# Kernel optimization log

Measured on AMD Instinct MI355X. Metric: run time of the kernel, lower is better.

Reference implementation:

```python
import jax, jax.numpy as jnp
import numpy as np

T_STEP, NUM_PATCHES = 16, 49
DIM, MLP_DIM, HEADS, DEPTH = 512, 2048, 8, 4
PATCH_DIM = 432
N_BATCH = 32
NEG = -1e9
EPS = 1e-5


def _ln(x, g, b):
    m = x.mean(-1, keepdims=True)
    v = ((x - m) ** 2).mean(-1, keepdims=True)
    return (x - m) / jnp.sqrt(v + EPS) * g + b


def setup_inputs() -> dict:
    key = jax.random.key(0)
    ks = jax.random.split(key, 16)
    L = T_STEP * NUM_PATCHES
    s = 0.02
    return {
        "patch": jax.random.normal(ks[0], (N_BATCH, L, PATCH_DIM), jnp.float32),
        "done": jax.random.randint(ks[1], (N_BATCH, T_STEP - 1), 0, 2).astype(jnp.int32),
        "W_embed": jax.random.normal(ks[2], (PATCH_DIM, DIM), jnp.float32) * s,
        "b_embed": jnp.zeros((DIM,), jnp.float32),
        "spatial_embed": jax.random.normal(ks[3], (1, NUM_PATCHES, DIM), jnp.float32),
        "temporal_embed": jax.random.normal(ks[4], (1, T_STEP, DIM), jnp.float32),
        "ln1_g": jnp.ones((DEPTH, DIM), jnp.float32),
        "ln1_b": jnp.zeros((DEPTH, DIM), jnp.float32),
        "Wqkv": jax.random.normal(ks[5], (DEPTH, DIM, 3 * DIM), jnp.float32) * s,
        "bqkv": jnp.zeros((DEPTH, 3 * DIM), jnp.float32),
        "Wo": jax.random.normal(ks[6], (DEPTH, DIM, DIM), jnp.float32) * s,
        "bo": jnp.zeros((DEPTH, DIM), jnp.float32),
        "ln2_g": jnp.ones((DEPTH, DIM), jnp.float32),
        "ln2_b": jnp.zeros((DEPTH, DIM), jnp.float32),
        "W1": jax.random.normal(ks[7], (DEPTH, DIM, MLP_DIM), jnp.float32) * s,
        "b1": jnp.zeros((DEPTH, MLP_DIM), jnp.float32),
        "W2": jax.random.normal(ks[8], (DEPTH, MLP_DIM, DIM), jnp.float32) * s,
        "b2": jnp.zeros((DEPTH, DIM), jnp.float32),
        "out_g": jnp.ones((DIM,), jnp.float32),
        "out_b": jnp.zeros((DIM,), jnp.float32),
    }


def reference(patch, done, W_embed, b_embed, spatial_embed, temporal_embed,
              ln1_g, ln1_b, Wqkv, bqkv, Wo, bo, ln2_g, ln2_b,
              W1, b1, W2, b2, out_g, out_b):
    N, L, _ = patch.shape
    # patch embed + factored pos embed
    x = patch @ W_embed + b_embed
    pos = jnp.tile(spatial_embed, (1, T_STEP, 1)) + jnp.repeat(temporal_embed, NUM_PATCHES, axis=1)
    x = x + pos
    # episodic attention mask: done_mask[n,t] = 1 iff any done[n, c]==1 for c >= t
    d = done.astype(jnp.float32)  # (N, T-1)
    dm = (jnp.flip(jnp.cumsum(jnp.flip(d, 1), 1), 1) > 0).astype(jnp.float32)
    dm = jnp.concatenate([dm, jnp.zeros((N, 1), jnp.float32)], axis=1)  # (N, T)
    pm = jnp.repeat(dm, NUM_PATCHES, axis=1)  # (N, L)
    keep = 1.0 - pm
    mask = 1.0 - keep[:, :, None] * keep[:, None, :]  # (N, L, L); 1 = blocked
    bias = jnp.where(mask > 0.5, NEG, 0.0)[:, None, :, :]  # (N, 1, L, L)
    dh = DIM // HEADS
    scale = dh ** -0.5
    for i in range(DEPTH):
        h = _ln(x, ln1_g[i], ln1_b[i])
        qkv = h @ Wqkv[i] + bqkv[i]
        q, k, v = jnp.split(qkv, 3, axis=-1)
        q = q.reshape(N, L, HEADS, dh).transpose(0, 2, 1, 3)
        k = k.reshape(N, L, HEADS, dh).transpose(0, 2, 1, 3)
        v = v.reshape(N, L, HEADS, dh).transpose(0, 2, 1, 3)
        scores = jnp.einsum('nhqd,nhkd->nhqk', q, k) * scale + bias
        attn = jax.nn.softmax(scores, axis=-1)
        o = jnp.einsum('nhqk,nhkd->nhqd', attn, v)
        o = o.transpose(0, 2, 1, 3).reshape(N, L, DIM)
        x = x + (o @ Wo[i] + bo[i])
        h = _ln(x, ln2_g[i], ln2_b[i])
        x = x + (jax.nn.gelu(h @ W1[i] + b1[i], approximate=False) @ W2[i] + b2[i])
    return _ln(x, out_g, out_b)
```

## Files before the change

### kernel.cpp

```cpp
#include <hip/hip_runtime.h>
#include <math.h>

#define NB 32
#define LQ 784
#define LQP 832
#define DIM 512
#define HEADS 8
#define MLP 2048
#define KPAD 448
#define MROWS 25088

typedef __attribute__((ext_vector_type(8))) short s8v;
typedef __attribute__((ext_vector_type(4))) short s4v;
typedef __attribute__((ext_vector_type(4))) float f4v;

__device__ __forceinline__ short f2b(float f){
  unsigned u = __builtin_bit_cast(unsigned, f);
  u = (u + 0x7fffu + ((u >> 16) & 1u)) >> 16;
  return (short)u;
}
__device__ __forceinline__ float b2f(short s){
  unsigned u = ((unsigned)(unsigned short)s) << 16;
  return __builtin_bit_cast(float, u);
}

__device__ __forceinline__ void gll16(const short* g, short* l){
  __builtin_amdgcn_global_load_lds(
      (const __attribute__((address_space(1))) void*)g,
      (__attribute__((address_space(3))) void*)l, 16, 0, 0);
}

__global__ __launch_bounds__(512) void mask_k(const int* __restrict__ done, float* __restrict__ keepL,
                                              int* __restrict__ kmask, int* __restrict__ liveg){
  __shared__ float keep[32][16];
  int tid = threadIdx.x;
  { int n = tid >> 4, t = tid & 15;
    int any = 0;
    for (int c = t; c < 15; ++c) any |= done[n*15 + c];
    keep[n][t] = any ? 0.f : 1.f; }
  __syncthreads();
  for (int i = tid; i < NB*LQP; i += 512){
    int n = i / LQP, l = i - n*LQP;
    keepL[i] = (l < LQ) ? keep[n][l/49] : 0.f;
  }
  if (tid < 32){
    int n = tid, m = 0;
    for (int kb = 0; kb < 13; ++kb){
      int t0 = (kb*64)/49, t1 = (kb*64 + 63)/49; if (t1 > 15) t1 = 15;
      float a = 0.f;
      for (int t = t0; t <= t1; ++t) a += keep[n][t];
      if (a > 0.5f) m |= 1 << kb;
    }
    kmask[n] = m;
  }
  for (int g = tid; g < 392; g += 512){
    float a = 0.f;
    for (int i2 = 0; i2 < 64; ++i2){
      int row = g*64 + i2;
      int n = row / 784, l = row - n*784;
      a += keep[n][l/49];
    }
    liveg[g] = a > 0.5f ? 1 : 0;
  }
}

__global__ __launch_bounds__(256) void zpad_k(short* __restrict__ Qb, short* __restrict__ Kb,
                                              short* __restrict__ Vtb){
  int idx = blockIdx.x*256 + threadIdx.x;
  s8v z;
  #pragma unroll
  for (int e=0;e<8;++e) z[e] = 0;
  if (idx < 98304){
    int nh = idx / 384, r = idx - nh*384;
    *(s8v*)(Qb + (long)nh*LQP*64 + 784*64 + r*8) = z;
  } else if (idx < 196608){
    int i2 = idx - 98304; int nh = i2 / 384, r = i2 - nh*384;
    *(s8v*)(Kb + (long)nh*LQP*64 + 784*64 + r*8) = z;
  } else {
    int i2 = idx - 196608; int nh = i2 / 384, rem = i2 - nh*384, d = rem/6, s = rem - d*6;
    *(s8v*)(Vtb + ((long)nh*64 + d)*LQP + 784 + s*8) = z;
  }
}

__global__ __launch_bounds__(256) void vmean_k(const short* __restrict__ Vtb, float* __restrict__ Vm){
  int nh = blockIdx.x;
  int tid = threadIdx.x;
  int d = tid >> 2, seg = tid & 3;
  const short* row = Vtb + ((long)nh*64 + d)*LQP;
  float s = 0.f;
  for (int c = seg; c < 98; c += 4){
    s8v v = *(const s8v*)(row + c*8);
    #pragma unroll
    for (int e=0;e<8;++e) s += b2f(v[e]);
  }
  s += __shfl_xor(s, 1, 64);
  s += __shfl_xor(s, 2, 64);
  if (seg == 0) Vm[nh*64 + d] = s * (1.0f/784.0f);
}

__device__ __forceinline__ void transp_body(long idx, const float* __restrict__ src,
                                            short* __restrict__ dst, int R, int C, int Rpad,
                                            long sStride, long dStride){
  long per = (long)C * Rpad;
  int z = (int)(idx / per);
  long rem = idx - (long)z * per;
  int cc = (int)(rem / Rpad);
  int r  = (int)(rem - (long)cc * Rpad);
  short v = 0;
  if (r < R) v = f2b(src[(long)z * sStride + (long)r * C + cc]);
  dst[(long)z * dStride + rem] = v;
}

#define PB0 43904
#define PB1 896
#define PB2 12288
#define PB3 4096
#define PB4 16384
#define PB5 16384

__global__ __launch_bounds__(256) void prep_k(
    const float* __restrict__ patch, short* __restrict__ patchb,
    const float* __restrict__ Wemb, short* __restrict__ Wembt,
    const float* __restrict__ Wqkv, short* __restrict__ Wqkvt,
    const float* __restrict__ Wo, short* __restrict__ Wot,
    const float* __restrict__ W1, short* __restrict__ W1t,
    const float* __restrict__ W2, short* __restrict__ W2t){
  int b = blockIdx.x;
  int tid = threadIdx.x;
  if (b < PB0){
    long idx = (long)b*256 + tid;
    if (idx >= (long)MROWS*KPAD) return;
    int r = (int)(idx / KPAD);
    int c = (int)(idx - (long)r*KPAD);
    patchb[idx] = (c < 432) ? f2b(patch[(long)r*432 + c]) : (short)0;
  } else if (b < PB0+PB1){
    long idx = (long)(b-PB0)*256 + tid;
    if (idx < 229376) transp_body(idx, Wemb, Wembt, 432, 512, 448, 0, 0);
  } else if (b < PB0+PB1+PB2){
    long idx = (long)(b-PB0-PB1)*256 + tid;
    if (idx < 3145728) transp_body(idx, Wqkv, Wqkvt, 512, 1536, 512, 512L*1536, 1536L*512);
  } else if (b < PB0+PB1+PB2+PB3){
    long idx = (long)(b-PB0-PB1-PB2)*256 + tid;
    if (idx < 1048576) transp_body(idx, Wo, Wot, 512, 512, 512, 512L*512, 512L*512);
  } else if (b < PB0+PB1+PB2+PB3+PB4){
    long idx = (long)(b-PB0-PB1-PB2-PB3)*256 + tid;
    if (idx < 4194304) transp_body(idx, W1, W1t, 512, 2048, 512, 512L*2048, 2048L*512);
  } else {
    long idx = (long)(b-PB0-PB1-PB2-PB3-PB4)*256 + tid;
    if (idx < 4194304) transp_body(idx, W2, W2t, 2048, 512, 2048, 2048L*512, 512L*2048);
  }
}

__global__ __launch_bounds__(256) void ln_k(const float* __restrict__ x, const float* __restrict__ g,
                                            const float* __restrict__ b, short* __restrict__ outb,
                                            float* __restrict__ outf){
  int lane = threadIdx.x & 63;
  long row = (long)blockIdx.x * 4 + (threadIdx.x >> 6);
  const float* xr = x + row * DIM + lane * 8;
  float va[8];
  { float4 t0 = *(const float4*)xr; float4 t1 = *(const float4*)(xr + 4);
    va[0]=t0.x; va[1]=t0.y; va[2]=t0.z; va[3]=t0.w;
    va[4]=t1.x; va[5]=t1.y; va[6]=t1.z; va[7]=t1.w; }
  float s = 0.f, q = 0.f;
  #pragma unroll
  for (int j=0;j<8;++j){ s += va[j]; q += va[j]*va[j]; }
  #pragma unroll
  for (int m=1;m<64;m<<=1){ s += __shfl_xor(s,m,64); q += __shfl_xor(q,m,64); }
  float mean = s * (1.0f/DIM);
  float var = q * (1.0f/DIM) - mean*mean;
  float inv = rsqrtf(var + 1e-5f);
  int cb = lane*8;
  if (outb){
    s8v o;
    #pragma unroll
    for (int j=0;j<8;++j) o[j] = f2b((va[j]-mean)*inv*g[cb+j] + b[cb+j]);
    *(s8v*)(outb + row*DIM + cb) = o;
  } else {
    float4 t0, t1;
    t0.x=(va[0]-mean)*inv*g[cb+0]+b[cb+0]; t0.y=(va[1]-mean)*inv*g[cb+1]+b[cb+1];
    t0.z=(va[2]-mean)*inv*g[cb+2]+b[cb+2]; t0.w=(va[3]-mean)*inv*g[cb+3]+b[cb+3];
    t1.x=(va[4]-mean)*inv*g[cb+4]+b[cb+4]; t1.y=(va[5]-mean)*inv*g[cb+5]+b[cb+5];
    t1.z=(va[6]-mean)*inv*g[cb+6]+b[cb+6]; t1.w=(va[7]-mean)*inv*g[cb+7]+b[cb+7];
    *(float4*)(outf + row*DIM + cb) = t0;
    *(float4*)(outf + row*DIM + cb + 4) = t1;
  }
}

template<int EPI>
__global__ __launch_bounds__(256) void gemm_k(
    const short* __restrict__ A, const short* __restrict__ Bt,
    const float* __restrict__ bias, int K, int N,
    float* __restrict__ xres, short* __restrict__ outb,
    const float* __restrict__ sp, const float* __restrict__ tp)
{
  __shared__ __align__(16) short lA[2][128*64];
  __shared__ __align__(16) short lB[2][128*64];
  long bm = blockIdx.y, bn = blockIdx.x;
  int tid = threadIdx.x;
  int lane = tid & 63, wid = tid >> 6;
  int col = lane & 15, quad = lane >> 4;
  int wm = (wid >> 1) * 64, wn = (wid & 1) * 64;
  f4v acc[4][4];
  #pragma unroll
  for (int i=0;i<4;++i)
    #pragma unroll
    for (int j=0;j<4;++j)
      #pragma unroll
      for (int e=0;e<4;++e) acc[i][j][e] = 0.0f;
  const short* Abase = A + bm*128*(long)K;
  const short* Bbase = Bt + bn*128*(long)K;
  int nt = K >> 6;
  #pragma unroll
  for (int c = 0; c < 4; ++c){
    int v = c*256 + tid;
    int r = v >> 3, j = v & 7;
    int kc = (j ^ (r & 7)) * 8;
    gll16(Abase + (long)r*K + kc, lA[0] + v*8);
    gll16(Bbase + (long)r*K + kc, lB[0] + v*8);
  }
  for (int t = 0; t < nt; ++t){
    int cur = t & 1;
    __builtin_amdgcn_s_barrier();
    __builtin_amdgcn_sched_barrier(0);
    if (t + 1 < nt){
      int kt = (t + 1) << 6;
      #pragma unroll
      for (int c = 0; c < 4; ++c){
        int v = c*256 + tid;
        int r = v >> 3, j = v & 7;
        int kc = (j ^ (r & 7)) * 8;
        gll16(Abase + (long)r*K + kt + kc, lA[cur^1] + v*8);
        gll16(Bbase + (long)r*K + kt + kc, lB[cur^1] + v*8);
      }
      asm volatile("s_waitcnt vmcnt(8)" ::: "memory");
    } else {
      asm volatile("s_waitcnt vmcnt(0)" ::: "memory");
    }
    __builtin_amdgcn_s_barrier();
    __builtin_amdgcn_sched_barrier(0);
    __builtin_amdgcn_s_setprio(1);
    #pragma unroll
    for (int ks = 0; ks < 2; ++ks){
      s8v af[4], bf[4];
      #pragma unroll
      for (int j=0;j<4;++j)
        af[j] = *(const s8v*)&lA[cur][(wm + j*16 + col)*64 + (((ks*4+quad) ^ (col&7)))*8];
      #pragma unroll
      for (int i=0;i<4;++i)
        bf[i] = *(const s8v*)&lB[cur][(wn + i*16 + col)*64 + (((ks*4+quad) ^ (col&7)))*8];
      #pragma unroll
      for (int i=0;i<4;++i)
        #pragma unroll
        for (int j=0;j<4;++j)
          acc[i][j] = __builtin_amdgcn_mfma_f32_16x16x32_bf16(bf[i], af[j], acc[i][j], 0, 0, 0);
    }
    __builtin_amdgcn_s_setprio(0);
    __builtin_amdgcn_sched_barrier(0);
  }
  #pragma unroll
  for (int j=0;j<4;++j){
    int grow = (int)bm*128 + wm + j*16 + col;
    int l = 0, t = 0, p = 0;
    if (EPI == 0){ l = grow % LQ; t = l / 49; p = l - t*49; }
    #pragma unroll
    for (int i=0;i<4;++i){
      int gc0 = (int)bn*128 + wn + i*16 + quad*4;
      float4 b4 = *(const float4*)(bias + gc0);
      float v0 = acc[i][j][0] + b4.x;
      float v1 = acc[i][j][1] + b4.y;
      float v2 = acc[i][j][2] + b4.z;
      float v3 = acc[i][j][3] + b4.w;
      if (EPI == 0){
        float4 s4 = *(const float4*)(sp + p*DIM + gc0);
        float4 t4 = *(const float4*)(tp + t*DIM + gc0);
        float4 o; o.x = v0 + s4.x + t4.x; o.y = v1 + s4.y + t4.y;
        o.z = v2 + s4.z + t4.z; o.w = v3 + s4.w + t4.w;
        *(float4*)(xres + (long)grow*DIM + gc0) = o;
      } else {
        float4 xo = *(const float4*)(xres + (long)grow*DIM + gc0);
        xo.x += v0; xo.y += v1; xo.z += v2; xo.w += v3;
        *(float4*)(xres + (long)grow*DIM + gc0) = xo;
      }
    }
  }
}

template<int EPI>
__global__ __launch_bounds__(512) void gemm256_k(
    const short* __restrict__ A, const short* __restrict__ Bt,
    const float* __restrict__ bias, int K, int N,
    short* __restrict__ outb,
    short* __restrict__ Qb, short* __restrict__ Kb, short* __restrict__ Vtb,
    const int* __restrict__ liveg)
{
  __shared__ __align__(16) short lA[2][256*64];
  __shared__ __align__(16) short lB[2][256*64];
  long bm = blockIdx.y, bn = blockIdx.x;
  if (EPI == 1){
    if (bn < 4 && liveg[4*bm] == 0 && liveg[4*bm+1] == 0 &&
        liveg[4*bm+2] == 0 && liveg[4*bm+3] == 0) return;
  }
  int tid = threadIdx.x;
  int lane = tid & 63, wid = tid >> 6;
  int col = lane & 15, quad = lane >> 4;
  int wm = (wid >> 2) * 128;
  int wn = (wid & 3) * 64;
  f4v acc[4][8];
  #pragma unroll
  for (int i=0;i<4;++i)
    #pragma unroll
    for (int j=0;j<8;++j)
      #pragma unroll
      for (int e=0;e<4;++e) acc[i][j][e] = 0.0f;
  const short* Abase = A + bm*256*(long)K;
  const short* Bbase = Bt + bn*256*(long)K;
  int nt = K >> 6;
  #pragma unroll
  for (int c = 0; c < 4; ++c){
    int v = c*512 + tid;
    int r = v >> 3, j = v & 7;
    int kc = (j ^ (r & 7)) * 8;
    gll16(Abase + (long)r*K + kc, lA[0] + v*8);
    gll16(Bbase + (long)r*K + kc, lB[0] + v*8);
  }
  for (int t = 0; t < nt; ++t){
    int cur = t & 1;
    __builtin_amdgcn_s_barrier();
    __builtin_amdgcn_sched_barrier(0);
    if (t + 1 < nt){
      int kt = (t + 1) << 6;
      #pragma unroll
      for (int c = 0; c < 4; ++c){
        int v = c*512 + tid;
        int r = v >> 3, j = v & 7;
        int kc = (j ^ (r & 7)) * 8;
        gll16(Abase + (long)r*K + kt + kc, lA[cur^1] + v*8);
        gll16(Bbase + (long)r*K + kt + kc, lB[cur^1] + v*8);
      }
      asm volatile("s_waitcnt vmcnt(8)" ::: "memory");
    } else {
      asm volatile("s_waitcnt vmcnt(0)" ::: "memory");
    }
    __builtin_amdgcn_s_barrier();
    __builtin_amdgcn_sched_barrier(0);
    __builtin_amdgcn_s_setprio(1);
    #pragma unroll
    for (int ks = 0; ks < 2; ++ks){
      s8v af[8], bf[4];
      #pragma unroll
      for (int j=0;j<8;++j)
        af[j] = *(const s8v*)&lA[cur][(wm + j*16 + col)*64 + (((ks*4+quad) ^ (col&7)))*8];
      #pragma unroll
      for (int i=0;i<4;++i)
        bf[i] = *(const s8v*)&lB[cur][(wn + i*16 + col)*64 + (((ks*4+quad) ^ (col&7)))*8];
      #pragma unroll
      for (int i=0;i<4;++i)
        #pragma unroll
        for (int j=0;j<8;++j)
          acc[i][j] = __builtin_amdgcn_mfma_f32_16x16x32_bf16(bf[i], af[j], acc[i][j], 0, 0, 0);
    }
    __builtin_amdgcn_s_setprio(0);
    __builtin_amdgcn_sched_barrier(0);
  }
  #pragma unroll
  for (int j=0;j<8;++j){
    int grow = (int)bm*256 + wm + j*16 + col;
    int n = 0, l = 0;
    if (EPI == 1){ n = grow / LQ; l = grow - n*LQ; }
    #pragma unroll
    for (int i=0;i<4;++i){
      int gc0 = (int)bn*256 + wn + i*16 + quad*4;
      float4 b4 = *(const float4*)(bias + gc0);
      float v0 = acc[i][j][0] + b4.x;
      float v1 = acc[i][j][1] + b4.y;
      float v2 = acc[i][j][2] + b4.z;
      float v3 = acc[i][j][3] + b4.w;
      if (EPI == 1){
        if (gc0 < 512){
          int hh = gc0 >> 6, d0 = gc0 & 63;
          s4v o; o[0]=f2b(v0); o[1]=f2b(v1); o[2]=f2b(v2); o[3]=f2b(v3);
          *(s4v*)(Qb + (((long)(n*HEADS + hh))*LQP + l)*64 + d0) = o;
        } else if (gc0 < 1024){
          int c2 = gc0 - 512; int hh = c2 >> 6, d0 = c2 & 63;
          s4v o; o[0]=f2b(v0); o[1]=f2b(v1); o[2]=f2b(v2); o[3]=f2b(v3);
          *(s4v*)(Kb + (((long)(n*HEADS + hh))*LQP + l)*64 + d0) = o;
        } else {
          int c2 = gc0 - 1024; int hh = c2 >> 6, d0 = c2 & 63;
          long base = ((long)(n*HEADS + hh))*64;
          Vtb[(base + d0+0)*LQP + l] = f2b(v0);
          Vtb[(base + d0+1)*LQP + l] = f2b(v1);
          Vtb[(base + d0+2)*LQP + l] = f2b(v2);
          Vtb[(base + d0+3)*LQP + l] = f2b(v3);
        }
      } else {
        float g0 = v0 / (1.0f + __expf(-1.595769122f * v0 * (1.0f + 0.044715f*v0*v0)));
        float g1 = v1 / (1.0f + __expf(-1.595769122f * v1 * (1.0f + 0.044715f*v1*v1)));
        float g2 = v2 / (1.0f + __expf(-1.595769122f * v2 * (1.0f + 0.044715f*v2*v2)));
        float g3 = v3 / (1.0f + __expf(-1.595769122f * v3 * (1.0f + 0.044715f*v3*v3)));
        s4v o; o[0]=f2b(g0); o[1]=f2b(g1); o[2]=f2b(g2); o[3]=f2b(g3);
        *(s4v*)(outb + (long)grow*MLP + gc0) = o;
      }
    }
  }
}

__global__ __launch_bounds__(256) void attn_k(
    const short* __restrict__ Qb, const short* __restrict__ Kb,
    const short* __restrict__ Vtb, const float* __restrict__ keepL,
    const int* __restrict__ kmask, const float* __restrict__ Vm,
    short* __restrict__ Ob)
{
  __shared__ __align__(16) short lK[64*64];
  __shared__ __align__(16) short lV[64*64];
  __shared__ __align__(16) short lP[4][16*72];
  int tid = threadIdx.x;
  int lane = tid & 63, wid = tid >> 6;
  int col = lane & 15, quad = lane >> 4;
  int qb = blockIdx.x, h = blockIdx.y, n = blockIdx.z;
  long nh = (long)n*HEADS + h;
  int smask = kmask[n];
  int qr0 = qb*64 + wid*16;
  float vmv[4];
  #pragma unroll
  for (int j=0;j<4;++j) vmv[j] = Vm[nh*64 + j*16 + col];

  if (!((smask >> qb) & 1)){
    #pragma unroll
    for (int j=0;j<4;++j){
      short ov = f2b(vmv[j]);
      #pragma unroll
      for (int r=0;r<4;++r){
        int l = qr0 + quad*4 + r;
        if (l < LQ) Ob[((long)n*LQ + l)*DIM + h*64 + j*16 + col] = ov;
      }
    }
    return;
  }

  const float* kl = keepL + n*LQP;
  const short* qp = Qb + (nh*LQP + qr0 + col)*64 + quad*8;
  s8v aq0 = *(const s8v*)qp;
  s8v aq1 = *(const s8v*)(qp + 32);
  float keepA = kl[qr0 + col];
  if (keepA < 0.5f){
    #pragma unroll
    for (int e=0;e<8;++e){ aq0[e] = 0; aq1[e] = 0; }
  }
  float keepQ[4];
  #pragma unroll
  for (int r=0;r<4;++r) keepQ[r] = kl[qr0 + quad*4 + r];
  float kqs = keepQ[0] + keepQ[1] + keepQ[2] + keepQ[3];
  bool wlive = __ballot(kqs > 0.5f) != 0ull;
  float lsum[4] = {0.f,0.f,0.f,0.f};
  f4v Oacc[4];
  #pragma unroll
  for (int j=0;j<4;++j)
    #pragma unroll
    for (int e=0;e<4;++e) Oacc[j][e] = 0.0f;

  for (int kb = 0; kb < 13; ++kb){
    if (!((smask >> kb) & 1)) continue;
    int kbase = kb*64;
    __syncthreads();
    #pragma unroll
    for (int c = 0; c < 2; ++c){
      int v = c*256 + tid;
      int r = v >> 3, j = v & 7;
      int kc = (j ^ (r & 7)) * 8;
      gll16(Kb + (nh*LQP + kbase + r)*64 + kc, lK + v*8);
    }
    #pragma unroll
    for (int c = 0; c < 2; ++c){
      int v = c*256 + tid;
      int d = v >> 3, j = v & 7;
      int c8 = (j ^ (d & 7)) * 8;
      gll16(Vtb + (nh*64 + d)*LQP + kbase + c8, lV + v*8);
    }
    __syncthreads();
    if (!wlive) continue;
    float pm[4][4];
    #pragma unroll
    for (int ct = 0; ct < 4; ++ct){
      float keepK = kl[kbase + ct*16 + col];
      f4v s;
      #pragma unroll
      for (int e=0;e<4;++e) s[e] = 0.0f;
      #pragma unroll
      for (int ks = 0; ks < 2; ++ks){
        s8v bk = *(const s8v*)&lK[(ct*16 + col)*64 + (((ks*4+quad) ^ (col&7)))*8];
        if (keepK < 0.5f){
          #pragma unroll
          for (int e=0;e<8;++e) bk[e] = 0;
        }
        s = __builtin_amdgcn_mfma_f32_16x16x32_bf16(ks ? aq1 : aq0, bk, s, 0, 0, 0);
      }
      #pragma unroll
      for (int r=0;r<4;++r){
        float a = keepQ[r] * keepK;
        float t = fmaf(s[r], 0.125f, 10000.0f);
        float p = __expf(fmaf(a, t, -10000.0f));
        pm[ct][r] = p;
        lsum[r] += p;
      }
    }
    #pragma unroll
    for (int ct=0; ct<4; ++ct)
      #pragma unroll
      for (int r=0;r<4;++r)
        lP[wid][(quad*4 + r)*72 + ct*16 + col] = f2b(pm[ct][r]);
    #pragma unroll
    for (int j=0;j<4;++j){
      #pragma unroll
      for (int ks=0; ks<2; ++ks){
        s8v ap = *(const s8v*)&lP[wid][col*72 + ks*32 + quad*8];
        s8v bv = *(const s8v*)&lV[(j*16 + col)*64 + (((ks*4+quad) ^ (col&7)))*8];
        Oacc[j] = __builtin_amdgcn_mfma_f32_16x16x32_bf16(ap, bv, Oacc[j], 0, 0, 0);
      }
    }
  }
  #pragma unroll
  for (int m=1; m<16; m<<=1){
    #pragma unroll
    for (int r=0;r<4;++r) lsum[r] += __shfl_xor(lsum[r], m, 64);
  }
  float invl[4];
  #pragma unroll
  for (int r=0;r<4;++r) invl[r] = 1.0f / lsum[r];
  #pragma unroll
  for (int j=0;j<4;++j)
    #pragma unroll
    for (int r=0;r<4;++r){
      int l = qr0 + quad*4 + r;
      if (l < LQ){
        float val = keepQ[r] > 0.5f ? Oacc[j][r] * invl[r] : vmv[j];
        Ob[((long)n*LQ + l)*DIM + h*64 + j*16 + col] = f2b(val);
      }
    }
}

extern "C" void kernel_launch(void* const* d_in, const int* in_sizes, int n_in,
                              void* d_out, int out_size, void* d_ws, size_t ws_size,
                              hipStream_t stream) {
  const float* patch    = (const float*)d_in[0];
  const int*   done     = (const int*)d_in[1];
  const float* W_embed  = (const float*)d_in[2];
  const float* b_embed  = (const float*)d_in[3];
  const float* spatial  = (const float*)d_in[4];
  const float* temporal = (const float*)d_in[5];
  const float* ln1_g    = (const float*)d_in[6];
  const float* ln1_b    = (const float*)d_in[7];
  const float* Wqkv     = (const float*)d_in[8];
  const float* bqkv     = (const float*)d_in[9];
  const float* Wo       = (const float*)d_in[10];
  const float* bo       = (const float*)d_in[11];
  const float* ln2_g    = (const float*)d_in[12];
  const float* ln2_b    = (const float*)d_in[13];
  const float* W1       = (const float*)d_in[14];
  const float* b1       = (const float*)d_in[15];
  const float* W2       = (const float*)d_in[16];
  const float* b2       = (const float*)d_in[17];
  const float* out_g    = (const float*)d_in[18];
  const float* out_b    = (const float*)d_in[19];
  float* out = (float*)d_out;

  char* ws = (char*)d_ws;
  size_t off = 0;
  auto alloc = [&](size_t bytes)->char*{ char* p = ws + off; off += (bytes + 255) & ~(size_t)255; return p; };
  const size_t QKV_B = (size_t)NB*HEADS*LQP*64*2;
  float* x    = (float*)alloc((size_t)MROWS*DIM*4);
  short* hbuf = (short*)alloc((size_t)MROWS*DIM*2);
  char*  U    = alloc((size_t)MROWS*MLP*2);
  short* patchb = (short*)U;
  short* Qb   = (short*)U;
  short* Kbf  = (short*)(U + QKV_B);
  short* Vtb  = (short*)(U + 2*QKV_B);
  short* obuf = hbuf;
  short* mid  = (short*)U;
  short* Wembt = (short*)alloc((size_t)512*448*2);
  short* Wqkvt = (short*)alloc((size_t)4*1536*512*2);
  short* Wot   = (short*)alloc((size_t)4*512*512*2);
  short* W1t   = (short*)alloc((size_t)4*2048*512*2);
  short* W2t   = (short*)alloc((size_t)4*512*2048*2);
  float* keepL = (float*)alloc((size_t)NB*LQP*4);
  int*   kmask = (int*)alloc(NB*4);
  int*   liveg = (int*)alloc(392*4);
  float* Vm    = (float*)alloc((size_t)NB*HEADS*64*4);

  mask_k<<<1, 512, 0, stream>>>(done, keepL, kmask, liveg);
  prep_k<<<PB0+PB1+PB2+PB3+PB4+PB5, 256, 0, stream>>>(
      patch, patchb, W_embed, Wembt, Wqkv, Wqkvt, Wo, Wot, W1, W1t, W2, W2t);

  gemm_k<0><<<dim3(DIM/128, MROWS/128), 256, 0, stream>>>(
      patchb, Wembt, b_embed, KPAD, DIM, x, nullptr, spatial, temporal);

  zpad_k<<<1152, 256, 0, stream>>>(Qb, Kbf, Vtb);

  for (int i = 0; i < 4; ++i){
    ln_k<<<MROWS/4, 256, 0, stream>>>(x, ln1_g + i*DIM, ln1_b + i*DIM, hbuf, nullptr);
    gemm256_k<1><<<dim3(1536/256, MROWS/256), 512, 0, stream>>>(
        hbuf, Wqkvt + (size_t)i*1536*512, bqkv + (size_t)i*1536, DIM, 1536,
        nullptr, Qb, Kbf, Vtb, liveg);
    vmean_k<<<NB*HEADS, 256, 0, stream>>>(Vtb, Vm);
    attn_k<<<dim3(13, HEADS, NB), 256, 0, stream>>>(Qb, Kbf, Vtb, keepL, kmask, Vm, obuf);
    gemm_k<2><<<dim3(DIM/128, MROWS/128), 256, 0, stream>>>(
        obuf, Wot + (size_t)i*512*512, bo + (size_t)i*DIM, DIM, DIM,
        x, nullptr, nullptr, nullptr);
    ln_k<<<MROWS/4, 256, 0, stream>>>(x, ln2_g + i*DIM, ln2_b + i*DIM, hbuf, nullptr);
    gemm256_k<3><<<dim3(MLP/256, MROWS/256), 512, 0, stream>>>(
        hbuf, W1t + (size_t)i*2048*512, b1 + (size_t)i*MLP, DIM, MLP,
        mid, nullptr, nullptr, nullptr, nullptr);
    gemm_k<2><<<dim3(DIM/128, MROWS/128), 256, 0, stream>>>(
        mid, W2t + (size_t)i*512*2048, b2 + (size_t)i*DIM, MLP, DIM,
        x, nullptr, nullptr, nullptr);
  }
  ln_k<<<MROWS/4, 256, 0, stream>>>(x, out_g, out_b, nullptr, out);
}
```

Before: 1.674 ms.

## Split gemm256 staging into sub-phases and use it for the MLP down-projection

Reworks the 256x256 bf16 GEMM so each k-tile's A and B loads are issued in four half-tile stages, interleaved with MFMA sub-blocks. B fragments are held in registers across the sub-blocks, aiming for finer overlap of global loads and compute. Adds a residual-add epilogue and routes the W2 projection through this kernel instead of the 128-tile GEMM. The 256-wide tiles on N=512 yield fewer blocks than CUs, which may cost occupancy, and the extra barriers per k-tile add sync overhead.

```diff
diff --git a/kernel.cpp b/kernel.cpp
--- a/kernel.cpp
+++ b/kernel.cpp
@@ -289,12 +289,12 @@
 __global__ __launch_bounds__(512) void gemm256_k(
     const short* __restrict__ A, const short* __restrict__ Bt,
     const float* __restrict__ bias, int K, int N,
-    short* __restrict__ outb,
+    float* __restrict__ xres, short* __restrict__ outb,
     short* __restrict__ Qb, short* __restrict__ Kb, short* __restrict__ Vtb,
     const int* __restrict__ liveg)
 {
-  __shared__ __align__(16) short lA[2][256*64];
-  __shared__ __align__(16) short lB[2][256*64];
+  __shared__ __align__(16) short lA[2][2][128*64];
+  __shared__ __align__(16) short lB[2][2][128*64];
   long bm = blockIdx.y, bn = blockIdx.x;
   if (EPI == 1){
     if (bn < 4 && liveg[4*bm] == 0 && liveg[4*bm+1] == 0 &&
@@ -305,6 +305,9 @@
   int col = lane & 15, quad = lane >> 4;
   int wm = (wid >> 2) * 128;
   int wn = (wid & 3) * 64;
+  int mg = wid >> 2;
+  int bh = (wid & 3) >> 1;
+  int bl = wn & 64;
   f4v acc[4][8];
   #pragma unroll
   for (int i=0;i<4;++i)
@@ -315,53 +318,67 @@
   const short* Abase = A + bm*256*(long)K;
   const short* Bbase = Bt + bn*256*(long)K;
   int nt = K >> 6;
-  #pragma unroll
-  for (int c = 0; c < 4; ++c){
-    int v = c*512 + tid;
-    int r = v >> 3, j = v & 7;
-    int kc = (j ^ (r & 7)) * 8;
-    gll16(Abase + (long)r*K + kc, lA[0] + v*8);
-    gll16(Bbase + (long)r*K + kc, lB[0] + v*8);
-  }
-  for (int t = 0; t < nt; ++t){
-    int cur = t & 1;
-    __builtin_amdgcn_s_barrier();
-    __builtin_amdgcn_sched_barrier(0);
-    if (t + 1 < nt){
-      int kt = (t + 1) << 6;
-      #pragma unroll
-      for (int c = 0; c < 4; ++c){
-        int v = c*512 + tid;
-        int r = v >> 3, j = v & 7;
-        int kc = (j ^ (r & 7)) * 8;
-        gll16(Abase + (long)r*K + kt + kc, lA[cur^1] + v*8);
-        gll16(Bbase + (long)r*K + kt + kc, lB[cur^1] + v*8);
-      }
-      asm volatile("s_waitcnt vmcnt(8)" ::: "memory");
-    } else {
-      asm volatile("s_waitcnt vmcnt(0)" ::: "memory");
-    }
-    __builtin_amdgcn_s_barrier();
-    __builtin_amdgcn_sched_barrier(0);
-    __builtin_amdgcn_s_setprio(1);
-    #pragma unroll
-    for (int ks = 0; ks < 2; ++ks){
-      s8v af[8], bf[4];
-      #pragma unroll
-      for (int j=0;j<8;++j)
-        af[j] = *(const s8v*)&lA[cur][(wm + j*16 + col)*64 + (((ks*4+quad) ^ (col&7)))*8];
-      #pragma unroll
-      for (int i=0;i<4;++i)
-        bf[i] = *(const s8v*)&lB[cur][(wn + i*16 + col)*64 + (((ks*4+quad) ^ (col&7)))*8];
-      #pragma unroll
-      for (int i=0;i<4;++i)
+  auto stageA = [&](int db, int h, int kt){
+    #pragma unroll
+    for (int c = 0; c < 2; ++c){
+      int v = c*512 + tid;
+      int r = v >> 3, j = v & 7;
+      int kc = (j ^ (r & 7)) * 8;
+      gll16(Abase + (long)(h*128 + r)*K + kt + kc, &lA[db][h][v*8]);
+    }
+  };
+  auto stageB = [&](int db, int h, int kt){
+    #pragma unroll
+    for (int c = 0; c < 2; ++c){
+      int v = c*512 + tid;
+      int r = v >> 3, j = v & 7;
+      int kc = (j ^ (r & 7)) * 8;
+      gll16(Bbase + (long)(h*128 + r)*K + kt + kc, &lB[db][h][v*8]);
+    }
+  };
+  stageA(0, 0, 0); stageA(0, 1, 0); stageB(0, 0, 0); stageB(0, 1, 0);
+  s8v bf[4][2];
+  for (int T = 0; T < nt; ++T){
+    int db = T & 1;
+    int ktn = (T + 1 < nt ? T + 1 : 0) << 6;
+    #pragma unroll
+    for (int q = 0; q < 4; ++q){
+      if (q == 0)      stageA(db^1, 0, ktn);
+      else if (q == 1) stageA(db^1, 1, ktn);
+      else if (q == 2) stageB(db^1, 0, ktn);
+      else             stageB(db^1, 1, ktn);
+      if (q == 0){
+        asm volatile("s_waitcnt vmcnt(2)" ::: "memory");
+        __builtin_amdgcn_s_barrier();
+        __builtin_amdgcn_sched_barrier(0);
         #pragma unroll
-        for (int j=0;j<8;++j)
-          acc[i][j] = __builtin_amdgcn_mfma_f32_16x16x32_bf16(bf[i], af[j], acc[i][j], 0, 0, 0);
-    }
-    __builtin_amdgcn_s_setprio(0);
-    __builtin_amdgcn_sched_barrier(0);
-  }
+        for (int i=0;i<4;++i)
+          #pragma unroll
+          for (int ks=0;ks<2;++ks)
+            bf[i][ks] = *(const s8v*)&lB[db][bh][(bl + i*16 + col)*64 + (((ks*4+quad) ^ (col&7)))*8];
+      }
+      s8v af[2][2];
+      #pragma unroll
+      for (int jj=0;jj<2;++jj)
+        #pragma unroll
+        for (int ks=0;ks<2;++ks)
+          af[jj][ks] = *(const s8v*)&lA[db][mg][((q*2+jj)*16 + col)*64 + (((ks*4+quad) ^ (col&7)))*8];
+      asm volatile("s_waitcnt lgkmcnt(0)" ::: "memory");
+      __builtin_amdgcn_sched_barrier(0);
+      __builtin_amdgcn_s_setprio(1);
+      #pragma unroll
+      for (int ks=0;ks<2;++ks)
+        #pragma unroll
+        for (int i=0;i<4;++i)
+          #pragma unroll
+          for (int jj=0;jj<2;++jj)
+            acc[i][q*2+jj] = __builtin_amdgcn_mfma_f32_16x16x32_bf16(bf[i][ks], af[jj][ks], acc[i][q*2+jj], 0, 0, 0);
+      __builtin_amdgcn_s_setprio(0);
+      __builtin_amdgcn_sched_barrier(0);
+      __builtin_amdgcn_s_barrier();
+    }
+  }
+  asm volatile("s_waitcnt vmcnt(0)" ::: "memory");
   #pragma unroll
   for (int j=0;j<8;++j){
     int grow = (int)bm*256 + wm + j*16 + col;
@@ -392,6 +409,10 @@
           Vtb[(base + d0+2)*LQP + l] = f2b(v2);
           Vtb[(base + d0+3)*LQP + l] = f2b(v3);
         }
+      } else if (EPI == 2){
+        float4 xo = *(const float4*)(xres + (long)grow*DIM + gc0);
+        xo.x += v0; xo.y += v1; xo.z += v2; xo.w += v3;
+        *(float4*)(xres + (long)grow*DIM + gc0) = xo;
       } else {
         float g0 = v0 / (1.0f + __expf(-1.595769122f * v0 * (1.0f + 0.044715f*v0*v0)));
         float g1 = v1 / (1.0f + __expf(-1.595769122f * v1 * (1.0f + 0.044715f*v1*v1)));
@@ -599,7 +620,7 @@
     ln_k<<<MROWS/4, 256, 0, stream>>>(x, ln1_g + i*DIM, ln1_b + i*DIM, hbuf, nullptr);
     gemm256_k<1><<<dim3(1536/256, MROWS/256), 512, 0, stream>>>(
         hbuf, Wqkvt + (size_t)i*1536*512, bqkv + (size_t)i*1536, DIM, 1536,
-        nullptr, Qb, Kbf, Vtb, liveg);
+        nullptr, nullptr, Qb, Kbf, Vtb, liveg);
     vmean_k<<<NB*HEADS, 256, 0, stream>>>(Vtb, Vm);
     attn_k<<<dim3(13, HEADS, NB), 256, 0, stream>>>(Qb, Kbf, Vtb, keepL, kmask, Vm, obuf);
     gemm_k<2><<<dim3(DIM/128, MROWS/128), 256, 0, stream>>>(
@@ -608,10 +629,10 @@
     ln_k<<<MROWS/4, 256, 0, stream>>>(x, ln2_g + i*DIM, ln2_b + i*DIM, hbuf, nullptr);
     gemm256_k<3><<<dim3(MLP/256, MROWS/256), 512, 0, stream>>>(
         hbuf, W1t + (size_t)i*2048*512, b1 + (size_t)i*MLP, DIM, MLP,
-        mid, nullptr, nullptr, nullptr, nullptr);
-    gemm_k<2><<<dim3(DIM/128, MROWS/128), 256, 0, stream>>>(
+        nullptr, mid, nullptr, nullptr, nullptr, nullptr);
+    gemm256_k<2><<<dim3(DIM/256, MROWS/256), 512, 0, stream>>>(
         mid, W2t + (size_t)i*512*2048, b2 + (size_t)i*DIM, MLP, DIM,
-        x, nullptr, nullptr, nullptr);
+        x, nullptr, nullptr, nullptr, nullptr, nullptr);
   }
   ln_k<<<MROWS/4, 256, 0, stream>>>(x, out_g, out_b, nullptr, out);
 }
```

After: 1.906 ms. 13.8% more time.
